# Kernel tuning notes

Hardware: AMD Instinct MI355X
Metric: run time of the kernel (lower is better)

Reference implementation:

```python
import jax, jax.numpy as jnp
import numpy as np

H = 10          # hidden_size
TAIL = 1440     # slice out[:, -1440:-1, :]


def _cell(x, h, c, w_ih, w_hh, b):
    # PyTorch LSTM gate order: i, f, g, o
    gates = x @ w_ih.T + h @ w_hh.T + b          # [B, 4H]
    i, f, g, o = jnp.split(gates, 4, axis=-1)
    c = jax.nn.sigmoid(f) * c + jax.nn.sigmoid(i) * jnp.tanh(g)
    h = jax.nn.sigmoid(o) * jnp.tanh(c)
    return h, c


def setup_inputs() -> dict:
    key = jax.random.key(0)
    ks = jax.random.split(key, 13)
    s = 1.0 / np.sqrt(H)  # PyTorch default init range

    def u(k, shape):
        return jax.random.uniform(k, shape, jnp.float32, -s, s)

    return {
        "x": jax.random.normal(ks[0], (4096, 2048), jnp.float32),
        "w_ih0": u(ks[1], (4 * H, 1)),
        "w_hh0": u(ks[2], (4 * H, H)),
        "b_ih0": u(ks[3], (4 * H,)),
        "b_hh0": u(ks[4], (4 * H,)),
        "w_ih1": u(ks[5], (4 * H, H)),
        "w_hh1": u(ks[6], (4 * H, H)),
        "b_ih1": u(ks[7], (4 * H,)),
        "b_hh1": u(ks[8], (4 * H,)),
        "fc1_w": u(ks[9], (6, H)),
        "fc1_b": u(ks[10], (6,)),
        "fc2_w": u(ks[11], (1, 6)),
        "fc2_b": u(ks[12], (1,)),
    }


def reference(x, w_ih0, w_hh0, b_ih0, b_hh0, w_ih1, w_hh1, b_ih1, b_hh1,
              fc1_w, fc1_b, fc2_w, fc2_b):
    B, T = x.shape
    xt = x[..., None].transpose(1, 0, 2)         # [T, B, 1] time-major
    b0 = b_ih0 + b_hh0
    b1 = b_ih1 + b_hh1
    z = jnp.zeros((B, H), x.dtype)

    def step(carry, xi):
        h0, c0, h1, c1 = carry
        h0, c0 = _cell(xi, h0, c0, w_ih0, w_hh0, b0)
        h1, c1 = _cell(h0, h1, c1, w_ih1, w_hh1, b1)
        return (h0, c0, h1, c1), h1

    _, ys = jax.lax.scan(step, (z, z, z, z), xt)  # ys: [T, B, H]
    out = ys.transpose(1, 0, 2)[:, T - TAIL:T - 1, :]   # [B, 1439, H]
    out = jnp.tanh(out @ fc1_w.T + fc1_b)                # [B, 1439, 6]
    out = out @ fc2_w.T + fc2_b                          # [B, 1439, 1]
    return out[..., 0]                                   # [B, 1439]
```

## Files before the change

kernel.cpp:

```cpp
#include <hip/hip_runtime.h>

typedef float v2f __attribute__((ext_vector_type(2)));

#define T_LEN 2048
#define NH    10
#define OUT_T 1439
#define TFIRST 608
#define NSEQ  4096
#define CH    16
#define NCH   (T_LEN / CH)
#define MFIRST (TFIRST / CH)

#define KSIG (-1.4426950408889634f)
#define KTAN (-2.8853900817779268f)

static __device__ __forceinline__ v2f fma2(v2f a, v2f b, v2f c) {
  return __builtin_elementwise_fma(a, b, c);
}
static __device__ __forceinline__ v2f splat2(float v) { v2f r; r.x = v; r.y = v; return r; }
static __device__ __forceinline__ v2f mulsp(v2f a, float s) { v2f r; r.x = a.x*s; r.y = a.y*s; return r; }
static __device__ __forceinline__ float rcp1p(float e) {
  return __builtin_amdgcn_rcpf(1.0f + e);
}

#define ROR_F(v, N) __uint_as_float(__builtin_amdgcn_update_dpp( \
    0, (int)__float_as_uint(v), 0x120 + (N), 0xF, 0xF, true))

__global__ void __launch_bounds__(128, 2)
lstm_fused(const float* __restrict__ x,
           const float* __restrict__ w_ih0, const float* __restrict__ w_hh0,
           const float* __restrict__ b_ih0, const float* __restrict__ b_hh0,
           const float* __restrict__ w_ih1, const float* __restrict__ w_hh1,
           const float* __restrict__ b_ih1, const float* __restrict__ b_hh1,
           const float* __restrict__ fc1_w, const float* __restrict__ fc1_b,
           const float* __restrict__ fc2_w, const float* __restrict__ fc2_b,
           float* __restrict__ out)
{
  __shared__ __align__(16) float h0buf[2][CH][64];
  __shared__ __align__(16) float h1buf[2][CH][64];

  const int tid  = threadIdx.x;
  const int wid  = tid >> 6;
  const int lane = tid & 63;
  const int grp  = lane >> 4;
  const int u    = lane & 15;
  const int seq  = (int)blockIdx.x * 4 + grp;

  v2f wIF[NH], wGO[NH], vIF[NH], vGO[NH];
  v2f wx_if, wx_go, bb_if, bb_go;
  wx_if = wx_go = bb_if = bb_go = splat2(0.f);
#pragma unroll
  for (int j = 0; j < NH; ++j) {
    wIF[j] = splat2(0.f); wGO[j] = splat2(0.f);
    vIF[j] = splat2(0.f); vGO[j] = splat2(0.f);
  }
  float fcw[NH];
#pragma unroll
  for (int j = 0; j < NH; ++j) fcw[j] = 0.f;
  float fcb = 0.f, fc2w2 = 0.f, fc2wn = 0.f;
  const float fc2bl = fc2_b[0];

  if (wid == 0) {
    if (u < NH) {
      const int ri = 0*NH+u, rf = 1*NH+u, rg = 2*NH+u, ro = 3*NH+u;
      wx_if.x = KSIG * w_ih0[ri];            wx_if.y = KSIG * w_ih0[rf];
      wx_go.x = KTAN * w_ih0[rg];            wx_go.y = KSIG * w_ih0[ro];
      bb_if.x = KSIG * (b_ih0[ri] + b_hh0[ri]); bb_if.y = KSIG * (b_ih0[rf] + b_hh0[rf]);
      bb_go.x = KTAN * (b_ih0[rg] + b_hh0[rg]); bb_go.y = KSIG * (b_ih0[ro] + b_hh0[ro]);
#pragma unroll
      for (int j = 0; j < NH; ++j) {
        wIF[j].x = KSIG * w_hh0[ri*NH+j]; wIF[j].y = KSIG * w_hh0[rf*NH+j];
        wGO[j].x = KTAN * w_hh0[rg*NH+j]; wGO[j].y = KSIG * w_hh0[ro*NH+j];
      }
    }
    if (u < 6) {
      fcb = KTAN * fc1_b[u];
      const float w2 = fc2_w[u];
      fc2w2 = 2.f * w2; fc2wn = -w2;
#pragma unroll
      for (int j = 0; j < NH; ++j) fcw[j] = KTAN * fc1_w[u*NH + j];
    }
  } else {
    if (u < NH) {
      const int ri = 0*NH+u, rf = 1*NH+u, rg = 2*NH+u, ro = 3*NH+u;
      bb_if.x = KSIG * (b_ih1[ri] + b_hh1[ri]); bb_if.y = KSIG * (b_ih1[rf] + b_hh1[rf]);
      bb_go.x = KTAN * (b_ih1[rg] + b_hh1[rg]); bb_go.y = KSIG * (b_ih1[ro] + b_hh1[ro]);
#pragma unroll
      for (int j = 0; j < NH; ++j) {
        wIF[j].x = KSIG * w_ih1[ri*NH+j]; wIF[j].y = KSIG * w_ih1[rf*NH+j];
        wGO[j].x = KTAN * w_ih1[rg*NH+j]; wGO[j].y = KSIG * w_ih1[ro*NH+j];
        vIF[j].x = KSIG * w_hh1[ri*NH+j]; vIF[j].y = KSIG * w_hh1[rf*NH+j];
        vGO[j].x = KTAN * w_hh1[rg*NH+j]; vGO[j].y = KSIG * w_hh1[ro*NH+j];
      }
    }
  }

  const float* xp   = x + (size_t)seq * T_LEN;
  float*       outp = out + (size_t)seq * OUT_T;

  float c = 0.f;
  float r0=0.f,r1=0.f,r2=0.f,r3=0.f,r4=0.f,r5=0.f,r6=0.f,r7=0.f,r8=0.f,r9=0.f;

  auto act_tail = [&](v2f gif, v2f ggo) -> float {
    const float ei = __builtin_amdgcn_exp2f(gif.x);
    const float ef = __builtin_amdgcn_exp2f(gif.y);
    const float eg = __builtin_amdgcn_exp2f(ggo.x);
    const float eo = __builtin_amdgcn_exp2f(ggo.y);
    const float sf = rcp1p(ef);
    const float ai = 1.0f + ei;
    const float d1 = __builtin_fmaf(ai, eg, ai);
    const float r1_ = __builtin_amdgcn_rcpf(d1);
    const float num = __builtin_fmaf(-KTAN, eg, KTAN);
    c = __builtin_fmaf(sf, c, num * r1_);
    const float cc = __builtin_fminf(__builtin_fmaxf(c, -64.f), 64.f);
    const float ec = __builtin_amdgcn_exp2f(cc);
    const float ao = 1.0f + eo;
    const float d2 = __builtin_fmaf(ao, ec, ao);
    const float r2_ = __builtin_amdgcn_rcpf(d2);
    return __builtin_fmaf(-ec, r2_, r2_);
  };

  auto a_chunk = [&](int m) {
    float* hb = &h0buf[m & 1][0][0];
    const float* hr = &h0buf[m & 1][0][grp * 16];
    const float4* xq = (const float4*)(xp + m * CH);
    float4 xw[CH / 4];
#pragma unroll
    for (int i = 0; i < CH / 4; ++i) xw[i] = xq[i];
#pragma unroll
    for (int s = 0; s < CH; ++s) {
      const float xv = ((const float*)xw)[s];
      v2f aA = fma2(wx_if, splat2(xv), bb_if);
      v2f gA = fma2(wx_go, splat2(xv), bb_go);
      v2f aB = mulsp(wIF[1], r1);
      v2f gB = mulsp(wGO[1], r1);
#define L0T(j, hv, AC, GC) { const v2f sp = splat2(hv); \
      AC = fma2(wIF[j], sp, AC); GC = fma2(wGO[j], sp, GC); }
      L0T(0,r0,aA,gA) L0T(2,r2,aA,gA) L0T(3,r3,aB,gB) L0T(4,r4,aA,gA)
      L0T(5,r5,aB,gB) L0T(6,r6,aA,gA) L0T(7,r7,aB,gB) L0T(8,r8,aA,gA)
      L0T(9,r9,aB,gB)
#undef L0T
      const float h0n = act_tail(aA + aB, gA + gB);
      hb[s*64 + lane] = h0n;
      const float4 va = *(const float4*)(hr + s*64);
      const float4 vb = *(const float4*)(hr + s*64 + 4);
      const float2 vc = *(const float2*)(hr + s*64 + 8);
      r0=va.x; r1=va.y; r2=va.z; r3=va.w;
      r4=vb.x; r5=vb.y; r6=vb.z; r7=vb.w;
      r8=vc.x; r9=vc.y;
    }
  };

  auto b_chunk = [&](int m) {
    const float* hbi = &h0buf[m & 1][0][grp * 16];
    float* ob = &h1buf[m & 1][0][0];
    const float* orr = &h1buf[m & 1][0][grp * 16];
#pragma unroll
    for (int s = 0; s < CH; ++s) {
      const float4 pa = *(const float4*)(hbi + s*64);
      const float4 pb = *(const float4*)(hbi + s*64 + 4);
      const float2 pc = *(const float2*)(hbi + s*64 + 8);
      v2f cA = fma2(wIF[0], splat2(pa.x), bb_if);
      v2f hA = fma2(wGO[0], splat2(pa.x), bb_go);
      v2f cB = mulsp(wIF[1], pa.y);
      v2f hB = mulsp(wGO[1], pa.y);
#define L1I(j, hv, AC, GC) { const v2f sp = splat2(hv); \
      AC = fma2(wIF[j], sp, AC); GC = fma2(wGO[j], sp, GC); }
      L1I(2,pa.z,cA,hA) L1I(3,pa.w,cB,hB) L1I(4,pb.x,cA,hA) L1I(5,pb.y,cB,hB)
      L1I(6,pb.z,cA,hA) L1I(7,pb.w,cB,hB) L1I(8,pc.x,cA,hA) L1I(9,pc.y,cB,hB)
#undef L1I
      v2f cC = mulsp(vIF[0], r0);
      v2f hC = mulsp(vGO[0], r0);
      v2f cD = mulsp(vIF[1], r1);
      v2f hD = mulsp(vGO[1], r1);
#define L1R(j, hv, AC, GC) { const v2f sp = splat2(hv); \
      AC = fma2(vIF[j], sp, AC); GC = fma2(vGO[j], sp, GC); }
      L1R(2,r2,cC,hC) L1R(3,r3,cD,hD) L1R(4,r4,cC,hC) L1R(5,r5,cD,hD)
      L1R(6,r6,cC,hC) L1R(7,r7,cD,hD) L1R(8,r8,cC,hC) L1R(9,r9,cD,hD)
#undef L1R
      const float h1n = act_tail((cA + cB) + (cC + cD), (hA + hB) + (hC + hD));
      ob[s*64 + lane] = h1n;
      const float4 va = *(const float4*)(orr + s*64);
      const float4 vb = *(const float4*)(orr + s*64 + 4);
      const float2 vc = *(const float2*)(orr + s*64 + 8);
      r0=va.x; r1=va.y; r2=va.z; r3=va.w;
      r4=vb.x; r5=vb.y; r6=vb.z; r7=vb.w;
      r8=vc.x; r9=vc.y;
    }
  };

  auto fc_chunk = [&](int m) {
    const float* hb = &h1buf[m & 1][0][grp * 16];
    float* oq = outp + (m * CH - TFIRST);
#pragma unroll
    for (int s = 0; s < CH; ++s) {
      if (m * CH + s < TFIRST + OUT_T) {
        const float4 pa = *(const float4*)(hb + s*64);
        const float4 pb = *(const float4*)(hb + s*64 + 4);
        const float2 pc = *(const float2*)(hb + s*64 + 8);
        float acc = __builtin_fmaf(pa.x, fcw[0], fcb);
        acc = __builtin_fmaf(pa.y, fcw[1], acc);
        acc = __builtin_fmaf(pa.z, fcw[2], acc);
        acc = __builtin_fmaf(pa.w, fcw[3], acc);
        acc = __builtin_fmaf(pb.x, fcw[4], acc);
        acc = __builtin_fmaf(pb.y, fcw[5], acc);
        acc = __builtin_fmaf(pb.z, fcw[6], acc);
        acc = __builtin_fmaf(pb.w, fcw[7], acc);
        acc = __builtin_fmaf(pc.x, fcw[8], acc);
        acc = __builtin_fmaf(pc.y, fcw[9], acc);
        const float rc = rcp1p(__builtin_amdgcn_exp2f(acc));
        float y = __builtin_fmaf(rc, fc2w2, fc2wn);
        y += ROR_F(y, 8);
        y += ROR_F(y, 4);
        y += ROR_F(y, 2);
        y += ROR_F(y, 1);
        if (u == 0) oq[s] = y + fc2bl;
      }
    }
  };

#pragma unroll 1
  for (int r = 0; r < NCH + 2; ++r) {
    if (wid == 0) {
      if (r < NCH) a_chunk(r);
      const int m = r - 2;
      if (m >= MFIRST && m < NCH) fc_chunk(m);
    } else {
      if (r >= 1 && r <= NCH) b_chunk(r - 1);
    }
    __syncthreads();
  }
}

extern "C" void kernel_launch(void* const* d_in, const int* in_sizes, int n_in,
                              void* d_out, int out_size, void* d_ws, size_t ws_size,
                              hipStream_t stream) {
  const float* x     = (const float*)d_in[0];
  const float* w_ih0 = (const float*)d_in[1];
  const float* w_hh0 = (const float*)d_in[2];
  const float* b_ih0 = (const float*)d_in[3];
  const float* b_hh0 = (const float*)d_in[4];
  const float* w_ih1 = (const float*)d_in[5];
  const float* w_hh1 = (const float*)d_in[6];
  const float* b_ih1 = (const float*)d_in[7];
  const float* b_hh1 = (const float*)d_in[8];
  const float* fc1_w = (const float*)d_in[9];
  const float* fc1_b = (const float*)d_in[10];
  const float* fc2_w = (const float*)d_in[11];
  const float* fc2_b = (const float*)d_in[12];
  float* out = (float*)d_out;

  lstm_fused<<<dim3(NSEQ / 4), dim3(128), 0, stream>>>(
      x, w_ih0, w_hh0, b_ih0, b_hh0, w_ih1, w_hh1, b_ih1, b_hh1,
      fc1_w, fc1_b, fc2_w, fc2_b, out);
}
```

Baseline: 688.5 us.

## Batch four chunks per barrier using an eight-slot LDS ring

Halves the chunk length and groups four chunks into each super-round, so the layer-0 wave, the layer-1 wave and the FC stage synchronise once every 32 timesteps instead of every 16. The hidden-state buffers become an eight-slot ring so producer and consumer chunks never share a slot within a super-round. This cuts barrier stalls and lets the two waves drift apart inside a super-round. In exchange it doubles LDS use and adds loop overhead from the non-unrolled inner chunk loops.

Result: slower. 709.9 us (+3.1%).

```diff
diff --git a/kernel.cpp b/kernel.cpp
--- a/kernel.cpp
+++ b/kernel.cpp
@@ -7,8 +7,11 @@
 #define OUT_T 1439
 #define TFIRST 608
 #define NSEQ  4096
-#define CH    16
+#define CH    8
 #define NCH   (T_LEN / CH)
+#define RING  8
+#define BPER  4
+#define NSR   (NCH / BPER + 2)
 #define MFIRST (TFIRST / CH)
 
 #define KSIG (-1.4426950408889634f)
@@ -36,8 +39,8 @@
            const float* __restrict__ fc2_w, const float* __restrict__ fc2_b,
            float* __restrict__ out)
 {
-  __shared__ __align__(16) float h0buf[2][CH][64];
-  __shared__ __align__(16) float h1buf[2][CH][64];
+  __shared__ __align__(16) float h0buf[RING][CH][64];
+  __shared__ __align__(16) float h1buf[RING][CH][64];
 
   const int tid  = threadIdx.x;
   const int wid  = tid >> 6;
@@ -121,8 +124,8 @@
   };
 
   auto a_chunk = [&](int m) {
-    float* hb = &h0buf[m & 1][0][0];
-    const float* hr = &h0buf[m & 1][0][grp * 16];
+    float* hb = &h0buf[m & (RING-1)][0][0];
+    const float* hr = hb + grp * 16;
     const float4* xq = (const float4*)(xp + m * CH);
     float4 xw[CH / 4];
 #pragma unroll
@@ -152,9 +155,9 @@
   };
 
   auto b_chunk = [&](int m) {
-    const float* hbi = &h0buf[m & 1][0][grp * 16];
-    float* ob = &h1buf[m & 1][0][0];
-    const float* orr = &h1buf[m & 1][0][grp * 16];
+    const float* hbi = &h0buf[m & (RING-1)][0][grp * 16];
+    float* ob = &h1buf[m & (RING-1)][0][0];
+    const float* orr = ob + grp * 16;
 #pragma unroll
     for (int s = 0; s < CH; ++s) {
       const float4 pa = *(const float4*)(hbi + s*64);
@@ -190,7 +193,7 @@
   };
 
   auto fc_chunk = [&](int m) {
-    const float* hb = &h1buf[m & 1][0][grp * 16];
+    const float* hb = &h1buf[m & (RING-1)][0][grp * 16];
     float* oq = outp + (m * CH - TFIRST);
 #pragma unroll
     for (int s = 0; s < CH; ++s) {
@@ -220,13 +223,24 @@
   };
 
 #pragma unroll 1
-  for (int r = 0; r < NCH + 2; ++r) {
+  for (int k = 0; k < NSR; ++k) {
     if (wid == 0) {
-      if (r < NCH) a_chunk(r);
-      const int m = r - 2;
-      if (m >= MFIRST && m < NCH) fc_chunk(m);
+      if (k < NCH / BPER) {
+#pragma unroll 1
+        for (int i = 0; i < BPER; ++i) a_chunk(k * BPER + i);
+      }
+      if (k >= 2) {
+#pragma unroll 1
+        for (int i = 0; i < BPER; ++i) {
+          const int m = (k - 2) * BPER + i;
+          if (m >= MFIRST && m < NCH) fc_chunk(m);
+        }
+      }
     } else {
-      if (r >= 1 && r <= NCH) b_chunk(r - 1);
+      if (k >= 1 && k <= NCH / BPER) {
+#pragma unroll 1
+        for (int i = 0; i < BPER; ++i) b_chunk((k - 1) * BPER + i);
+      }
     }
     __syncthreads();
   }
```

## Interleave two independent sequence groups per wave and prefetch next x chunk

Applied to the files above, without the earlier changes.

Each block now processes 8 sequences instead of 4, with every wave interleaving two independent LSTM recurrences step by step. The aim is to hide the serial dependency latency of each step (exp/rcp chains, LDS round-trips) through instruction-level parallelism across the two chains. It also prefetches the next chunk of x while computing the current one. The cost is doubled register and LDS usage, launch bounds lowered to one block per SIMD pair, and half as many blocks.

New measurement: 1.284 ms. +86.5%, slower.

```diff
diff --git a/kernel.cpp b/kernel.cpp
--- a/kernel.cpp
+++ b/kernel.cpp
@@ -26,7 +26,10 @@
 #define ROR_F(v, N) __uint_as_float(__builtin_amdgcn_update_dpp( \
     0, (int)__float_as_uint(v), 0x120 + (N), 0xF, 0xF, true))
 
-__global__ void __launch_bounds__(128, 2)
+#define XEL(a, s) (((s)&3)==0 ? a[(s)>>2].x : ((s)&3)==1 ? a[(s)>>2].y : \
+                   ((s)&3)==2 ? a[(s)>>2].z : a[(s)>>2].w)
+
+__global__ void __launch_bounds__(128, 1)
 lstm_fused(const float* __restrict__ x,
            const float* __restrict__ w_ih0, const float* __restrict__ w_hh0,
            const float* __restrict__ b_ih0, const float* __restrict__ b_hh0,
@@ -36,15 +39,15 @@
            const float* __restrict__ fc2_w, const float* __restrict__ fc2_b,
            float* __restrict__ out)
 {
-  __shared__ __align__(16) float h0buf[2][CH][64];
-  __shared__ __align__(16) float h1buf[2][CH][64];
+  __shared__ __align__(16) float h0buf[2][2][CH][64];
+  __shared__ __align__(16) float h1buf[2][2][CH][64];
 
   const int tid  = threadIdx.x;
   const int wid  = tid >> 6;
   const int lane = tid & 63;
   const int grp  = lane >> 4;
   const int u    = lane & 15;
-  const int seq  = (int)blockIdx.x * 4 + grp;
+  const int seq0 = (int)blockIdx.x * 8 + grp;
 
   v2f wIF[NH], wGO[NH], vIF[NH], vGO[NH];
   v2f wx_if, wx_go, bb_if, bb_go;
@@ -95,13 +98,16 @@
     }
   }
 
-  const float* xp   = x + (size_t)seq * T_LEN;
-  float*       outp = out + (size_t)seq * OUT_T;
-
-  float c = 0.f;
-  float r0=0.f,r1=0.f,r2=0.f,r3=0.f,r4=0.f,r5=0.f,r6=0.f,r7=0.f,r8=0.f,r9=0.f;
-
-  auto act_tail = [&](v2f gif, v2f ggo) -> float {
+  const float* xp0  = x + (size_t)seq0 * T_LEN;
+  const float* xp1  = xp0 + (size_t)4 * T_LEN;
+  float*       op0  = out + (size_t)seq0 * OUT_T;
+  float*       op1  = op0 + (size_t)4 * OUT_T;
+
+  float cg0 = 0.f, cg1 = 0.f;
+  float p0=0.f,p1=0.f,p2=0.f,p3=0.f,p4=0.f,p5=0.f,p6=0.f,p7=0.f,p8=0.f,p9=0.f;
+  float q0=0.f,q1=0.f,q2=0.f,q3=0.f,q4=0.f,q5=0.f,q6=0.f,q7=0.f,q8=0.f,q9=0.f;
+
+  auto act_tail = [&](float& c, v2f gif, v2f ggo) -> float {
     const float ei = __builtin_amdgcn_exp2f(gif.x);
     const float ef = __builtin_amdgcn_exp2f(gif.y);
     const float eg = __builtin_amdgcn_exp2f(ggo.x);
@@ -120,78 +126,66 @@
     return __builtin_fmaf(-ec, r2_, r2_);
   };
 
-  auto a_chunk = [&](int m) {
-    float* hb = &h0buf[m & 1][0][0];
-    const float* hr = &h0buf[m & 1][0][grp * 16];
-    const float4* xq = (const float4*)(xp + m * CH);
-    float4 xw[CH / 4];
-#pragma unroll
-    for (int i = 0; i < CH / 4; ++i) xw[i] = xq[i];
-#pragma unroll
-    for (int s = 0; s < CH; ++s) {
-      const float xv = ((const float*)xw)[s];
-      v2f aA = fma2(wx_if, splat2(xv), bb_if);
-      v2f gA = fma2(wx_go, splat2(xv), bb_go);
-      v2f aB = mulsp(wIF[1], r1);
-      v2f gB = mulsp(wGO[1], r1);
+  auto l0_step = [&](float xv, float& c,
+                     float& m0, float& m1, float& m2, float& m3, float& m4,
+                     float& m5, float& m6, float& m7, float& m8, float& m9,
+                     float* hb, const float* hr, int s) {
+    v2f aA = fma2(wx_if, splat2(xv), bb_if);
+    v2f gA = fma2(wx_go, splat2(xv), bb_go);
+    v2f aB = mulsp(wIF[1], m1);
+    v2f gB = mulsp(wGO[1], m1);
 #define L0T(j, hv, AC, GC) { const v2f sp = splat2(hv); \
-      AC = fma2(wIF[j], sp, AC); GC = fma2(wGO[j], sp, GC); }
-      L0T(0,r0,aA,gA) L0T(2,r2,aA,gA) L0T(3,r3,aB,gB) L0T(4,r4,aA,gA)
-      L0T(5,r5,aB,gB) L0T(6,r6,aA,gA) L0T(7,r7,aB,gB) L0T(8,r8,aA,gA)
-      L0T(9,r9,aB,gB)
+    AC = fma2(wIF[j], sp, AC); GC = fma2(wGO[j], sp, GC); }
+    L0T(0,m0,aA,gA) L0T(2,m2,aA,gA) L0T(3,m3,aB,gB) L0T(4,m4,aA,gA)
+    L0T(5,m5,aB,gB) L0T(6,m6,aA,gA) L0T(7,m7,aB,gB) L0T(8,m8,aA,gA)
+    L0T(9,m9,aB,gB)
 #undef L0T
-      const float h0n = act_tail(aA + aB, gA + gB);
-      hb[s*64 + lane] = h0n;
-      const float4 va = *(const float4*)(hr + s*64);
-      const float4 vb = *(const float4*)(hr + s*64 + 4);
-      const float2 vc = *(const float2*)(hr + s*64 + 8);
-      r0=va.x; r1=va.y; r2=va.z; r3=va.w;
-      r4=vb.x; r5=vb.y; r6=vb.z; r7=vb.w;
-      r8=vc.x; r9=vc.y;
-    }
-  };
-
-  auto b_chunk = [&](int m) {
-    const float* hbi = &h0buf[m & 1][0][grp * 16];
-    float* ob = &h1buf[m & 1][0][0];
-    const float* orr = &h1buf[m & 1][0][grp * 16];
-#pragma unroll
-    for (int s = 0; s < CH; ++s) {
-      const float4 pa = *(const float4*)(hbi + s*64);
-      const float4 pb = *(const float4*)(hbi + s*64 + 4);
-      const float2 pc = *(const float2*)(hbi + s*64 + 8);
-      v2f cA = fma2(wIF[0], splat2(pa.x), bb_if);
-      v2f hA = fma2(wGO[0], splat2(pa.x), bb_go);
-      v2f cB = mulsp(wIF[1], pa.y);
-      v2f hB = mulsp(wGO[1], pa.y);
+    const float h0n = act_tail(c, aA + aB, gA + gB);
+    hb[s*64 + lane] = h0n;
+    const float4 va = *(const float4*)(hr + s*64);
+    const float4 vb = *(const float4*)(hr + s*64 + 4);
+    const float2 vc = *(const float2*)(hr + s*64 + 8);
+    m0=va.x; m1=va.y; m2=va.z; m3=va.w;
+    m4=vb.x; m5=vb.y; m6=vb.z; m7=vb.w;
+    m8=vc.x; m9=vc.y;
+  };
+
+  auto l1_step = [&](const float* hp, float& c,
+                     float& m0, float& m1, float& m2, float& m3, float& m4,
+                     float& m5, float& m6, float& m7, float& m8, float& m9,
+                     float* ob, const float* orr, int s) {
+    const float4 pa = *(const float4*)(hp);
+    const float4 pb = *(const float4*)(hp + 4);
+    const float2 pc = *(const float2*)(hp + 8);
+    v2f cA = fma2(wIF[0], splat2(pa.x), bb_if);
+    v2f hA = fma2(wGO[0], splat2(pa.x), bb_go);
+    v2f cB = mulsp(wIF[1], pa.y);
+    v2f hB = mulsp(wGO[1], pa.y);
 #define L1I(j, hv, AC, GC) { const v2f sp = splat2(hv); \
-      AC = fma2(wIF[j], sp, AC); GC = fma2(wGO[j], sp, GC); }
-      L1I(2,pa.z,cA,hA) L1I(3,pa.w,cB,hB) L1I(4,pb.x,cA,hA) L1I(5,pb.y,cB,hB)
-      L1I(6,pb.z,cA,hA) L1I(7,pb.w,cB,hB) L1I(8,pc.x,cA,hA) L1I(9,pc.y,cB,hB)
+    AC = fma2(wIF[j], sp, AC); GC = fma2(wGO[j], sp, GC); }
+    L1I(2,pa.z,cA,hA) L1I(3,pa.w,cB,hB) L1I(4,pb.x,cA,hA) L1I(5,pb.y,cB,hB)
+    L1I(6,pb.z,cA,hA) L1I(7,pb.w,cB,hB) L1I(8,pc.x,cA,hA) L1I(9,pc.y,cB,hB)
 #undef L1I
-      v2f cC = mulsp(vIF[0], r0);
-      v2f hC = mulsp(vGO[0], r0);
-      v2f cD = mulsp(vIF[1], r1);
-      v2f hD = mulsp(vGO[1], r1);
+    v2f cC = mulsp(vIF[0], m0);
+    v2f hC = mulsp(vGO[0], m0);
+    v2f cD = mulsp(vIF[1], m1);
+    v2f hD = mulsp(vGO[1], m1);
 #define L1R(j, hv, AC, GC) { const v2f sp = splat2(hv); \
-      AC = fma2(vIF[j], sp, AC); GC = fma2(vGO[j], sp, GC); }
-      L1R(2,r2,cC,hC) L1R(3,r3,cD,hD) L1R(4,r4,cC,hC) L1R(5,r5,cD,hD)
-      L1R(6,r6,cC,hC) L1R(7,r7,cD,hD) L1R(8,r8,cC,hC) L1R(9,r9,cD,hD)
+    AC = fma2(vIF[j], sp, AC); GC = fma2(vGO[j], sp, GC); }
+    L1R(2,m2,cC,hC) L1R(3,m3,cD,hD) L1R(4,m4,cC,hC) L1R(5,m5,cD,hD)
+    L1R(6,m6,cC,hC) L1R(7,m7,cD,hD) L1R(8,m8,cC,hC) L1R(9,m9,cD,hD)
 #undef L1R
-      const float h1n = act_tail((cA + cB) + (cC + cD), (hA + hB) + (hC + hD));
-      ob[s*64 + lane] = h1n;
-      const float4 va = *(const float4*)(orr + s*64);
-      const float4 vb = *(const float4*)(orr + s*64 + 4);
-      const float2 vc = *(const float2*)(orr + s*64 + 8);
-      r0=va.x; r1=va.y; r2=va.z; r3=va.w;
-      r4=vb.x; r5=vb.y; r6=vb.z; r7=vb.w;
-      r8=vc.x; r9=vc.y;
-    }
-  };
-
-  auto fc_chunk = [&](int m) {
-    const float* hb = &h1buf[m & 1][0][grp * 16];
-    float* oq = outp + (m * CH - TFIRST);
+    const float h1n = act_tail(c, (cA + cB) + (cC + cD), (hA + hB) + (hC + hD));
+    ob[s*64 + lane] = h1n;
+    const float4 va = *(const float4*)(orr + s*64);
+    const float4 vb = *(const float4*)(orr + s*64 + 4);
+    const float2 vc = *(const float2*)(orr + s*64 + 8);
+    m0=va.x; m1=va.y; m2=va.z; m3=va.w;
+    m4=vb.x; m5=vb.y; m6=vb.z; m7=vb.w;
+    m8=vc.x; m9=vc.y;
+  };
+
+  auto fc_one = [&](const float* hb, float* oq, int m) {
 #pragma unroll
     for (int s = 0; s < CH; ++s) {
       if (m * CH + s < TFIRST + OUT_T) {
@@ -219,14 +213,59 @@
     }
   };
 
+  float4 xc0[CH/4], xc1[CH/4];
+  if (wid == 0) {
+    const float4* a = (const float4*)xp0;
+    const float4* b = (const float4*)xp1;
+#pragma unroll
+    for (int i = 0; i < CH/4; ++i) { xc0[i] = a[i]; xc1[i] = b[i]; }
+  }
+
 #pragma unroll 1
   for (int r = 0; r < NCH + 2; ++r) {
     if (wid == 0) {
-      if (r < NCH) a_chunk(r);
+      if (r < NCH) {
+        float4 xn0[CH/4], xn1[CH/4];
+        if (r + 1 < NCH) {
+          const float4* a = (const float4*)(xp0 + (r+1) * CH);
+          const float4* b = (const float4*)(xp1 + (r+1) * CH);
+#pragma unroll
+          for (int i = 0; i < CH/4; ++i) { xn0[i] = a[i]; xn1[i] = b[i]; }
+        }
+        float* hb0 = &h0buf[r & 1][0][0][0];
+        float* hb1 = &h0buf[r & 1][1][0][0];
+        const float* hr0 = hb0 + grp * 16;
+        const float* hr1 = hb1 + grp * 16;
+#pragma unroll
+        for (int s = 0; s < CH; ++s) {
+          l0_step(XEL(xc0, s), cg0, p0,p1,p2,p3,p4,p5,p6,p7,p8,p9, hb0, hr0, s);
+          l0_step(XEL(xc1, s), cg1, q0,q1,q2,q3,q4,q5,q6,q7,q8,q9, hb1, hr1, s);
+        }
+        if (r + 1 < NCH) {
+#pragma unroll
+          for (int i = 0; i < CH/4; ++i) { xc0[i] = xn0[i]; xc1[i] = xn1[i]; }
+        }
+      }
       const int m = r - 2;
-      if (m >= MFIRST && m < NCH) fc_chunk(m);
+      if (m >= MFIRST && m < NCH) {
+        fc_one(&h1buf[m & 1][0][0][grp * 16], op0 + (m * CH - TFIRST), m);
+        fc_one(&h1buf[m & 1][1][0][grp * 16], op1 + (m * CH - TFIRST), m);
+      }
     } else {
-      if (r >= 1 && r <= NCH) b_chunk(r - 1);
+      const int m = r - 1;
+      if (m >= 0 && m < NCH) {
+        const float* hbi0 = &h0buf[m & 1][0][0][grp * 16];
+        const float* hbi1 = &h0buf[m & 1][1][0][grp * 16];
+        float* ob0 = &h1buf[m & 1][0][0][0];
+        float* ob1 = &h1buf[m & 1][1][0][0];
+        const float* or0 = ob0 + grp * 16;
+        const float* or1 = ob1 + grp * 16;
+#pragma unroll
+        for (int s = 0; s < CH; ++s) {
+          l1_step(hbi0 + s*64, cg0, p0,p1,p2,p3,p4,p5,p6,p7,p8,p9, ob0, or0, s);
+          l1_step(hbi1 + s*64, cg1, q0,q1,q2,q3,q4,q5,q6,q7,q8,q9, ob1, or1, s);
+        }
+      }
     }
     __syncthreads();
   }
@@ -250,7 +289,7 @@
   const float* fc2_b = (const float*)d_in[12];
   float* out = (float*)d_out;
 
-  lstm_fused<<<dim3(NSEQ / 4), dim3(128), 0, stream>>>(
+  lstm_fused<<<dim3(NSEQ / 8), dim3(128), 0, stream>>>(
       x, w_ih0, w_hh0, b_ih0, b_hh0, w_ih1, w_hh1, b_ih1, b_hh1,
       fc1_w, fc1_b, fc2_w, fc2_b, out);
 }
```
